# Optimization experiments

Measured on AMD Instinct MI355X. Metric: run time of the kernel, lower is better.

The kernel has to match this reference:

```python
import jax, jax.numpy as jnp
import numpy as np

B, N, OBS, H, A = 1024, 64, 128, 256, 16
NH = 4
HD = H // NH


def _linear_params(key, fan_in, fan_out):
    k1, k2 = jax.random.split(key)
    bound = 1.0 / np.sqrt(fan_in)
    W = jax.random.uniform(k1, (fan_out, fan_in), jnp.float32, -bound, bound)
    b = jax.random.uniform(k2, (fan_out,), jnp.float32, -bound, bound)
    return W, b


def setup_inputs() -> dict:
    key = jax.random.key(0)
    ks = jax.random.split(key, 10)
    obs = jax.random.normal(ks[0], (B, N, OBS), jnp.float32)
    adj = jax.random.randint(ks[1], (B, N, N), 0, 2).astype(jnp.float32)
    # guarantee every row has at least one neighbor (self-loop) so softmax is finite
    adj = jnp.maximum(adj, jnp.eye(N, dtype=jnp.float32)[None])
    W1, b1 = _linear_params(ks[2], OBS, H)
    W2, b2 = _linear_params(ks[3], H, H)
    Wq, bq = _linear_params(ks[4], H, H)
    Wk, bk = _linear_params(ks[5], H, H)
    Wv, bv = _linear_params(ks[6], H, H)
    Wo, bo = _linear_params(ks[7], H, H)
    Wc, bc = _linear_params(ks[8], H, H)
    W3, b3 = _linear_params(ks[9], H, A)
    return dict(obs=obs, adj=adj, W1=W1, b1=b1, W2=W2, b2=b2,
                Wq=Wq, bq=bq, Wk=Wk, bk=bk, Wv=Wv, bv=bv,
                Wo=Wo, bo=bo, Wc=Wc, bc=bc, W3=W3, b3=b3)


def reference(obs, adj, W1, b1, W2, b2, Wq, bq, Wk, bk, Wv, bv, Wo, bo, Wc, bc, W3, b3):
    lin = lambda x, W, b: jnp.einsum('bnd,od->bno', x, W) + b
    x = jax.nn.relu(lin(obs, W1, b1))
    x = jax.nn.relu(lin(x, W2, b2))
    # multi-head attention with adjacency mask
    def heads(t):  # [B,N,H] -> [B,NH,N,HD]
        return t.reshape(B, N, NH, HD).transpose(0, 2, 1, 3)
    q = heads(lin(x, Wq, bq))
    k = heads(lin(x, Wk, bk))
    v = heads(lin(x, Wv, bv))
    scores = jnp.einsum('bhqd,bhkd->bhqk', q, k) / np.sqrt(HD).astype(np.float32)
    scores = jnp.where(adj[:, None] == 0, -jnp.inf, scores)
    attn = jax.nn.softmax(scores, axis=-1)
    out = jnp.einsum('bhqk,bhkd->bhqd', attn, v)
    out = out.transpose(0, 2, 1, 3).reshape(B, N, H)
    x = lin(out, Wo, bo)
    # communication: adj @ fc(x)
    x = jnp.einsum('bnm,bmh->bnh', adj, lin(x, Wc, bc))
    return lin(x, W3, b3)
```

## Files before the change

kernel.cpp:

```cpp
#include <hip/hip_runtime.h>
#include <stdint.h>

typedef unsigned short u16;
typedef unsigned long long u64;
typedef __attribute__((ext_vector_type(8))) short short8;
typedef __attribute__((ext_vector_type(4))) float f32x4;

#define MFMA16 __builtin_amdgcn_mfma_f32_16x16x32_bf16

#define B_ 1024
#define N_ 64
#define MTOT (B_ * N_)

__device__ __forceinline__ u16 f2bf(float f) {
  union { float f; uint32_t u; } v; v.f = f;
  uint32_t r = v.u + 0x7FFFu + ((v.u >> 16) & 1u);
  return (u16)(r >> 16);
}

union U8 { short8 v; u16 u[8]; };
union U4 { u64 v; u16 u[4]; };

__device__ __forceinline__ void cp16(const void* g, void* l) {
  __builtin_amdgcn_global_load_lds(
      (const __attribute__((address_space(1))) void*)g,
      (__attribute__((address_space(3))) void*)l, 16, 0, 0);
}

__global__ __launch_bounds__(256) void k_l1(
    const float* __restrict__ obs, u16* __restrict__ obsb,
    const float* __restrict__ Wc, const float* __restrict__ Wo,
    const float* __restrict__ bo, const float* __restrict__ bc,
    float* __restrict__ M1, float* __restrict__ bv,
    const float* __restrict__ W1, const float* __restrict__ W2,
    const float* __restrict__ Wq, const float* __restrict__ Wk,
    u16* o1, u16* o2, u16* oq, u16* ok) {
  const int bid = blockIdx.x, tid = threadIdx.x;
  if (bid < 4096) {
    const int e = (bid * 256 + tid) * 8;
    f32x4 a = *(const f32x4*)(obs + e);
    f32x4 b = *(const f32x4*)(obs + e + 4);
    U8 pk;
#pragma unroll
    for (int j = 0; j < 4; j++) { pk.u[j] = f2bf(a[j]); pk.u[4 + j] = f2bf(b[j]); }
    *(short8*)(obsb + e) = pk.v;
  } else if (bid < 4352) {
    __shared__ float wcr[256];
    __shared__ float red[4];
    const int j = bid - 4096, d = tid;
    wcr[d] = Wc[j * 256 + d];
    __syncthreads();
    float acc = 0.f;
    for (int i = 0; i < 256; i++) acc += wcr[i] * Wo[i * 256 + d];
    M1[j * 256 + d] = acc;
    float p = wcr[d] * bo[d];
    for (int off = 32; off >= 1; off >>= 1) p += __shfl_xor(p, off);
    if ((d & 63) == 0) red[d >> 6] = p;
    __syncthreads();
    if (d == 0) bv[j] = bc[j] + red[0] + red[1] + red[2] + red[3];
  } else {
    int off8 = (bid - 4352) * 256 + tid;
    const float* src; u16* dst;
    if      (off8 <  4096) { src = W1; dst = o1; }
    else if (off8 < 12288) { src = W2; dst = o2; off8 -= 4096; }
    else if (off8 < 20480) { src = Wq; dst = oq; off8 -= 12288; }
    else                   { src = Wk; dst = ok; off8 -= 20480; }
    const int e = off8 * 8;
    f32x4 a = *(const f32x4*)(src + e);
    f32x4 b = *(const f32x4*)(src + e + 4);
    U8 pk;
#pragma unroll
    for (int j = 0; j < 4; j++) { pk.u[j] = f2bf(a[j]); pk.u[4 + j] = f2bf(b[j]); }
    *(short8*)(dst + e) = pk.v;
  }
}

template<int K>
__device__ __forceinline__ void gemm128t(
    const u16* __restrict__ A, const u16* __restrict__ W,
    const float* __restrict__ bias, u16* __restrict__ C,
    const int m0, const int n0, const bool relu, char* smem) {
  char* As = smem;
  char* Bs = smem + 16384;
  const int tid = threadIdx.x;
  const int lane = tid & 63, wid = tid >> 6;
  const int wr = wid >> 1, wc = wid & 1;
  const int ro = lane & 15, hi = lane >> 4;

  f32x4 acc[4][4];
#pragma unroll
  for (int m = 0; m < 4; m++)
#pragma unroll
    for (int n = 0; n < 4; n++) acc[m][n] = (f32x4){0.f, 0.f, 0.f, 0.f};

  for (int k0 = 0; k0 < K; k0 += 64) {
#pragma unroll
    for (int i = 0; i < 4; i++) {
      const int boff = i * 4096 + wid * 1024;
      const int t = boff + lane * 16;
      const int row = t >> 7;
      const int cb = (t & 127) ^ ((row & 7) << 4);
      cp16(A + (size_t)(m0 + row) * K + k0 + (cb >> 1), As + boff);
    }
#pragma unroll
    for (int i = 0; i < 4; i++) {
      const int boff = i * 4096 + wid * 1024;
      const int t = boff + lane * 16;
      const int row = t >> 7;
      const int cb = (t & 127) ^ ((row & 7) << 4);
      cp16(W + (size_t)(n0 + row) * K + k0 + (cb >> 1), Bs + boff);
    }
    __syncthreads();
#pragma unroll
    for (int kk = 0; kk < 64; kk += 32) {
      short8 af[4], bfr[4];
#pragma unroll
      for (int m = 0; m < 4; m++) {
        const int row = wr * 64 + m * 16 + ro;
        af[m] = *(const short8*)(As + ((row * 128 + (kk + hi * 8) * 2) ^ ((row & 7) << 4)));
      }
#pragma unroll
      for (int n = 0; n < 4; n++) {
        const int row = wc * 64 + n * 16 + ro;
        bfr[n] = *(const short8*)(Bs + ((row * 128 + (kk + hi * 8) * 2) ^ ((row & 7) << 4)));
      }
#pragma unroll
      for (int m = 0; m < 4; m++)
#pragma unroll
        for (int n = 0; n < 4; n++)
          acc[m][n] = MFMA16(af[m], bfr[n], acc[m][n], 0, 0, 0);
    }
    __syncthreads();
  }

  u16 (*Cs)[136] = (u16(*)[136])smem;
#pragma unroll
  for (int half = 0; half < 2; half++) {
    if (wr == half) {
#pragma unroll
      for (int n = 0; n < 4; n++) {
        const int col = wc * 64 + n * 16 + ro;
        const float bb = bias[n0 + col];
#pragma unroll
        for (int m = 0; m < 4; m++)
#pragma unroll
          for (int j = 0; j < 4; j++) {
            float val = acc[m][n][j] + bb;
            if (relu) val = fmaxf(val, 0.f);
            Cs[m * 16 + hi * 4 + j][col] = f2bf(val);
          }
      }
    }
    __syncthreads();
    for (int i = tid; i < 64 * 16; i += 256) {
      const int r = i >> 4, c = (i & 15) << 3;
      *(short8*)(C + (size_t)(m0 + half * 64 + r) * 256 + n0 + c) = *(short8*)&Cs[r][c];
    }
    __syncthreads();
  }
}

__global__ __launch_bounds__(256, 4) void k_gemm1_prep2(
    const u16* __restrict__ obsb, const u16* __restrict__ W1b,
    const float* __restrict__ b1, u16* __restrict__ x1,
    const float* __restrict__ W3, const float* __restrict__ M1,
    const float* __restrict__ bvchain, const float* __restrict__ bvw,
    float* __restrict__ Wzf, float* __restrict__ bz) {
  __shared__ char smem[32768];
  if (blockIdx.x < 1024) {
    gemm128t<128>(obsb, W1b, b1, x1, (int)(blockIdx.x >> 1) * 128,
                  (int)(blockIdx.x & 1) * 128, true, smem);
    return;
  }
  float* w3r = (float*)smem;
  float* red = (float*)(smem + 1024);
  const int a = blockIdx.x - 1024, d = threadIdx.x;
  w3r[d] = W3[a * 256 + d];
  __syncthreads();
  float acc = 0.f;
  for (int j = 0; j < 256; j++) acc += w3r[j] * M1[j * 256 + d];
  Wzf[a * 256 + d] = acc;
  float p = w3r[d] * bvchain[d] + acc * bvw[d];
  for (int off = 32; off >= 1; off >>= 1) p += __shfl_xor(p, off);
  if ((d & 63) == 0) red[d >> 6] = p;
  __syncthreads();
  if (d == 0) bz[a] = red[0] + red[1] + red[2] + red[3];
}

__global__ __launch_bounds__(256, 4) void k_x2_prep3(
    const u16* __restrict__ x1, const u16* __restrict__ W2b,
    const float* __restrict__ b2, u16* __restrict__ x2,
    const float* __restrict__ Wzf, const float* __restrict__ Wv,
    u16* __restrict__ G) {
  __shared__ char smem[32768];
  if (blockIdx.x < 1024) {
    gemm128t<256>(x1, W2b, b2, x2, (int)(blockIdx.x >> 1) * 128,
                  (int)(blockIdx.x & 1) * 128, true, smem);
    return;
  }
  const int g = blockIdx.x - 1024, d2 = threadIdx.x;
  const int h = g >> 4, a = g & 15;
  float* wzr = (float*)smem;
  if (d2 < 64) wzr[d2] = Wzf[a * 256 + h * 64 + d2];
  __syncthreads();
  float acc = 0.f;
#pragma unroll 8
  for (int d = 0; d < 64; d++) acc += wzr[d] * Wv[(size_t)(h * 64 + d) * 256 + d2];
  G[g * 256 + d2] = f2bf(acc);
}

__global__ __launch_bounds__(256, 4) void k_qk_gemmv(
    const u16* __restrict__ x2,
    const u16* __restrict__ Wqb, const float* __restrict__ bq, u16* __restrict__ Qg,
    const u16* __restrict__ Wkb, const float* __restrict__ bk, u16* __restrict__ Kg,
    const u16* __restrict__ G, u16* __restrict__ Vzt) {
  __shared__ char smem[32768];
  const int bid = blockIdx.x;
  if (bid < 2048) {
    const int which = bid & 1;
    gemm128t<256>(x2, which ? Wkb : Wqb, which ? bk : bq, which ? Kg : Qg,
                  (bid >> 2) * 128, ((bid >> 1) & 1) * 128, false, smem);
    return;
  }
  char* As = smem;
  char* Bs = smem + 16384;
  const int tid = threadIdx.x;
  const int lane = tid & 63, w = tid >> 6;
  const int ro = lane & 15, hi = lane >> 4;
  const int m0 = (bid - 2048) * 128;

  f32x4 acc[2][4];
#pragma unroll
  for (int m = 0; m < 2; m++)
#pragma unroll
    for (int n = 0; n < 4; n++) acc[m][n] = (f32x4){0.f, 0.f, 0.f, 0.f};

  for (int k0 = 0; k0 < 256; k0 += 64) {
#pragma unroll
    for (int i = 0; i < 4; i++) {
      const int boff = i * 4096 + w * 1024;
      const int t = boff + lane * 16;
      const int row = t >> 7;
      const int cb = (t & 127) ^ ((row & 7) << 4);
      cp16(x2 + (size_t)(m0 + row) * 256 + k0 + (cb >> 1), As + boff);
    }
    {
      const int boff = w * 1024;
      const int t = boff + lane * 16;
      const int row = t >> 7;
      const int cb = (t & 127) ^ ((row & 7) << 4);
      cp16(G + (size_t)row * 256 + k0 + (cb >> 1), Bs + boff);
      const int boff2 = 4096 + w * 1024;
      const int t2 = boff2 + lane * 16;
      const int row2 = t2 >> 7;
      const int cb2 = (t2 & 127) ^ ((row2 & 7) << 4);
      cp16(G + (size_t)row2 * 256 + k0 + (cb2 >> 1), Bs + boff2);
    }
    __syncthreads();
#pragma unroll
    for (int kk = 0; kk < 64; kk += 32) {
      short8 af[2], bfr[4];
#pragma unroll
      for (int m = 0; m < 2; m++) {
        const int row = w * 32 + m * 16 + ro;
        af[m] = *(const short8*)(As + ((row * 128 + (kk + hi * 8) * 2) ^ ((row & 7) << 4)));
      }
#pragma unroll
      for (int n = 0; n < 4; n++) {
        const int row = n * 16 + ro;
        bfr[n] = *(const short8*)(Bs + ((row * 128 + (kk + hi * 8) * 2) ^ ((row & 7) << 4)));
      }
#pragma unroll
      for (int m = 0; m < 2; m++)
#pragma unroll
        for (int n = 0; n < 4; n++)
          acc[m][n] = MFMA16(af[m], bfr[n], acc[m][n], 0, 0, 0);
    }
    __syncthreads();
  }

#pragma unroll
  for (int m = 0; m < 2; m++) {
    const int rbase = w * 32 + m * 16;
    const int bidx = (m0 >> 6) + (rbase >> 6);
    const int ke = (rbase + hi * 4) & 63;
#pragma unroll
    for (int n = 0; n < 4; n++) {
      const int c = n * 16 + ro;
      U4 pk;
#pragma unroll
      for (int j = 0; j < 4; j++) pk.u[j] = f2bf(acc[m][n][j]);
      *(u64*)(Vzt + (size_t)bidx * 4096 + (size_t)c * 64 + ke) = pk.v;
    }
  }
}

__global__ __launch_bounds__(256, 2) void attn_fused(
    const u16* __restrict__ Qg, const u16* __restrict__ Kg,
    const u16* __restrict__ Vzt, const float* __restrict__ adj,
    const float* __restrict__ bz, const float* __restrict__ b3,
    float* __restrict__ out) {
  __shared__ u16 Ps[4][64][72];
  __shared__ float Zs[4][64][16];
  __shared__ u64 adjm[64];
  __shared__ u16 chunk[64][4];

  const int b = blockIdx.x, tid = threadIdx.x;
  const int lane = tid & 63, w = tid >> 6;
  const int ro = lane & 15, hi = lane >> 4;
  const int hc = w * 64;
  const size_t base = (size_t)b * 64 * 256;

  short8 kb[4][2];
#pragma unroll
  for (int n = 0; n < 4; n++)
#pragma unroll
    for (int ks = 0; ks < 2; ks++)
      kb[n][ks] = *(const short8*)(Kg + base + (size_t)(n * 16 + ro) * 256 + hc + ks * 32 + hi * 8);

  {
    const int q = tid >> 2, qa = tid & 3;
    const float* ar = adj + ((size_t)b * 64 + q) * 64 + qa * 16;
    f32x4 a0 = *(const f32x4*)(ar);
    f32x4 a1 = *(const f32x4*)(ar + 4);
    f32x4 a2 = *(const f32x4*)(ar + 8);
    f32x4 a3 = *(const f32x4*)(ar + 12);
    unsigned m16 = 0;
#pragma unroll
    for (int i = 0; i < 4; i++) {
      m16 |= (unsigned)(a0[i] != 0.f) << i;
      m16 |= (unsigned)(a1[i] != 0.f) << (4 + i);
      m16 |= (unsigned)(a2[i] != 0.f) << (8 + i);
      m16 |= (unsigned)(a3[i] != 0.f) << (12 + i);
    }
    chunk[q][qa] = (u16)m16;
  }

  f32x4 s[4][4];
#pragma unroll
  for (int m = 0; m < 4; m++) {
    short8 af[2];
#pragma unroll
    for (int ks = 0; ks < 2; ks++)
      af[ks] = *(const short8*)(Qg + base + (size_t)(m * 16 + ro) * 256 + hc + ks * 32 + hi * 8);
#pragma unroll
    for (int n = 0; n < 4; n++) s[m][n] = (f32x4){0.f, 0.f, 0.f, 0.f};
#pragma unroll
    for (int ks = 0; ks < 2; ks++)
#pragma unroll
      for (int n = 0; n < 4; n++)
        s[m][n] = MFMA16(af[ks], kb[n][ks], s[m][n], 0, 0, 0);
  }

  short8 vz[2];
#pragma unroll
  for (int ks = 0; ks < 2; ks++)
    vz[ks] = *(const short8*)(Vzt + (size_t)b * 4096 + (size_t)(hc / 4 + ro) * 64 + ks * 32 + hi * 8);

  __syncthreads();
  if (tid < 64)
    adjm[tid] = (u64)chunk[tid][0] | ((u64)chunk[tid][1] << 16) |
                ((u64)chunk[tid][2] << 32) | ((u64)chunk[tid][3] << 48);
  __syncthreads();

#pragma unroll
  for (int m = 0; m < 4; m++) {
#pragma unroll
    for (int j = 0; j < 4; j++) {
      const int q = m * 16 + hi * 4 + j;
      const u64 msk = adjm[q];
      float sv[4], ev[4];
      float mx = -3.0e38f;
#pragma unroll
      for (int n = 0; n < 4; n++) {
        const bool on = (msk >> (n * 16 + ro)) & 1ull;
        sv[n] = on ? s[m][n][j] * 0.125f : -3.0e38f;
        mx = fmaxf(mx, sv[n]);
      }
      mx = fmaxf(mx, __shfl_xor(mx, 1));
      mx = fmaxf(mx, __shfl_xor(mx, 2));
      mx = fmaxf(mx, __shfl_xor(mx, 4));
      mx = fmaxf(mx, __shfl_xor(mx, 8));
      float sum = 0.f;
#pragma unroll
      for (int n = 0; n < 4; n++) {
        ev[n] = (sv[n] > -1.0e37f) ? __expf(sv[n] - mx) : 0.f;
        sum += ev[n];
      }
      sum += __shfl_xor(sum, 1);
      sum += __shfl_xor(sum, 2);
      sum += __shfl_xor(sum, 4);
      sum += __shfl_xor(sum, 8);
      const float inv = 1.0f / sum;
#pragma unroll
      for (int n = 0; n < 4; n++)
        Ps[w][q][n * 16 + ro] = f2bf(ev[n] * inv);
    }
  }

#pragma unroll
  for (int m = 0; m < 4; m++) {
    short8 pa[2];
    pa[0] = *(const short8*)&Ps[w][m * 16 + ro][hi * 8];
    pa[1] = *(const short8*)&Ps[w][m * 16 + ro][32 + hi * 8];
    f32x4 oz = (f32x4){0.f, 0.f, 0.f, 0.f};
#pragma unroll
    for (int ks = 0; ks < 2; ks++)
      oz = MFMA16(pa[ks], vz[ks], oz, 0, 0, 0);
#pragma unroll
    for (int j = 0; j < 4; j++)
      Zs[w][m * 16 + hi * 4 + j][ro] = oz[j];
  }
  __syncthreads();

  for (int i = tid; i < 1024; i += 256) {
    const int r = i >> 4, a = i & 15;
    Zs[0][r][a] += Zs[1][r][a] + Zs[2][r][a] + Zs[3][r][a];
  }
  __syncthreads();

  {
    const int n = tid >> 2, a4 = (tid & 3) << 2;
    const u64 msk = adjm[n];
    const float deg = (float)__popcll(msk);
    float a0 = 0.f, a1 = 0.f, a2 = 0.f, a3 = 0.f;
#pragma unroll 8
    for (int m = 0; m < 64; m++) {
      const float wv = (float)((msk >> m) & 1ull);
      f32x4 z = *(const f32x4*)&Zs[0][m][a4];
      a0 += wv * z[0]; a1 += wv * z[1]; a2 += wv * z[2]; a3 += wv * z[3];
    }
    f32x4 r;
    r[0] = a0 + b3[a4 + 0] + deg * bz[a4 + 0];
    r[1] = a1 + b3[a4 + 1] + deg * bz[a4 + 1];
    r[2] = a2 + b3[a4 + 2] + deg * bz[a4 + 2];
    r[3] = a3 + b3[a4 + 3] + deg * bz[a4 + 3];
    *(f32x4*)(out + ((size_t)b * 64 + n) * 16 + a4) = r;
  }
}

extern "C" void kernel_launch(void* const* d_in, const int* in_sizes, int n_in,
                              void* d_out, int out_size, void* d_ws, size_t ws_size,
                              hipStream_t stream) {
  const float* obs = (const float*)d_in[0];
  const float* adj = (const float*)d_in[1];
  const float* W1  = (const float*)d_in[2];
  const float* b1  = (const float*)d_in[3];
  const float* W2  = (const float*)d_in[4];
  const float* b2  = (const float*)d_in[5];
  const float* Wq  = (const float*)d_in[6];
  const float* bq  = (const float*)d_in[7];
  const float* Wk  = (const float*)d_in[8];
  const float* bk  = (const float*)d_in[9];
  const float* Wv  = (const float*)d_in[10];
  const float* bvw = (const float*)d_in[11];
  const float* Wo  = (const float*)d_in[12];
  const float* bo  = (const float*)d_in[13];
  const float* Wc  = (const float*)d_in[14];
  const float* bc  = (const float*)d_in[15];
  const float* W3  = (const float*)d_in[16];
  const float* b3  = (const float*)d_in[17];
  float* out = (float*)d_out;

  char* ws = (char*)d_ws;
  const size_t BIG = (size_t)MTOT * 256 * 2;
  u16* buf0 = (u16*)(ws);
  u16* buf1 = (u16*)(ws + BIG);
  u16* buf2 = (u16*)(ws + 2 * BIG);
  u16* buf3 = (u16*)(ws + 3 * BIG);
  char* p = ws + 4 * BIG;
  u16* W1b = (u16*)p;              p += 128 * 256 * 2;
  u16* W2b = (u16*)p;              p += 256 * 256 * 2;
  u16* Wqb = (u16*)p;              p += 256 * 256 * 2;
  u16* Wkb = (u16*)p;              p += 256 * 256 * 2;
  float* M1 = (float*)p;           p += 256 * 256 * 4;
  float* Wzf = (float*)p;          p += 16 * 256 * 4;
  u16* G   = (u16*)p;              p += 64 * 256 * 2;
  float* bv = (float*)p;           p += 256 * 4;
  float* bz = (float*)p;           p += 16 * 4;
  u16* obsb = (u16*)p;             p += (size_t)MTOT * 128 * 2;

  dim3 blk(256);
  k_l1<<<dim3(4464), blk, 0, stream>>>(obs, obsb, Wc, Wo, bo, bc, M1, bv,
                                       W1, W2, Wq, Wk, W1b, W2b, Wqb, Wkb);
  k_gemm1_prep2<<<dim3(1040), blk, 0, stream>>>(obsb, W1b, b1, buf0,
                                                W3, M1, bv, bvw, Wzf, bz);
  k_x2_prep3<<<dim3(1088), blk, 0, stream>>>(buf0, W2b, b2, buf1, Wzf, Wv, G);
  k_qk_gemmv<<<dim3(2560), blk, 0, stream>>>(buf1, Wqb, bq, buf2,
                                             Wkb, bk, buf3, G, buf0);
  attn_fused<<<dim3(1024), blk, 0, stream>>>(buf2, buf3, buf0, adj, bz, b3, out);
}
```

Measured before the change: 128.4 us.

## Widen GEMM tiles to full 256-column output so each block reuses the A tile

The bf16 GEMM helper now computes a 128x256 output tile per block, using two accumulator sets and two B tiles in LDS. Previously two blocks each loaded the same A rows for the two column halves. Block counts are halved, LDS per block grows to 48KB and launch bounds drop to 2 blocks per CU to fit the doubled accumulators. The Q/K GEMM blocks are also remapped so that Q and K work on the same row tiles sits close together, for L2 locality. The trade is less A traffic against lower occupancy and fewer blocks to spread across CUs.

```diff
diff --git a/kernel.cpp b/kernel.cpp
--- a/kernel.cpp
+++ b/kernel.cpp
@@ -76,22 +76,26 @@
 }
 
 template<int K>
-__device__ __forceinline__ void gemm128t(
+__device__ __forceinline__ void gemm_full(
     const u16* __restrict__ A, const u16* __restrict__ W,
     const float* __restrict__ bias, u16* __restrict__ C,
-    const int m0, const int n0, const bool relu, char* smem) {
-  char* As = smem;
-  char* Bs = smem + 16384;
+    const int m0, const bool relu, char* smem) {
+  char* As  = smem;
+  char* Bs0 = smem + 16384;
+  char* Bs1 = smem + 32768;
   const int tid = threadIdx.x;
   const int lane = tid & 63, wid = tid >> 6;
   const int wr = wid >> 1, wc = wid & 1;
   const int ro = lane & 15, hi = lane >> 4;
 
-  f32x4 acc[4][4];
+  f32x4 acc0[4][4], acc1[4][4];
 #pragma unroll
   for (int m = 0; m < 4; m++)
 #pragma unroll
-    for (int n = 0; n < 4; n++) acc[m][n] = (f32x4){0.f, 0.f, 0.f, 0.f};
+    for (int n = 0; n < 4; n++) {
+      acc0[m][n] = (f32x4){0.f, 0.f, 0.f, 0.f};
+      acc1[m][n] = (f32x4){0.f, 0.f, 0.f, 0.f};
+    }
 
   for (int k0 = 0; k0 < K; k0 += 64) {
 #pragma unroll
@@ -101,19 +105,13 @@
       const int row = t >> 7;
       const int cb = (t & 127) ^ ((row & 7) << 4);
       cp16(A + (size_t)(m0 + row) * K + k0 + (cb >> 1), As + boff);
-    }
-#pragma unroll
-    for (int i = 0; i < 4; i++) {
-      const int boff = i * 4096 + wid * 1024;
-      const int t = boff + lane * 16;
-      const int row = t >> 7;
-      const int cb = (t & 127) ^ ((row & 7) << 4);
-      cp16(W + (size_t)(n0 + row) * K + k0 + (cb >> 1), Bs + boff);
+      cp16(W + (size_t)row * K + k0 + (cb >> 1), Bs0 + boff);
+      cp16(W + (size_t)(128 + row) * K + k0 + (cb >> 1), Bs1 + boff);
     }
     __syncthreads();
 #pragma unroll
     for (int kk = 0; kk < 64; kk += 32) {
-      short8 af[4], bfr[4];
+      short8 af[4], b0[4], b1[4];
 #pragma unroll
       for (int m = 0; m < 4; m++) {
         const int row = wr * 64 + m * 16 + ro;
@@ -122,59 +120,66 @@
 #pragma unroll
       for (int n = 0; n < 4; n++) {
         const int row = wc * 64 + n * 16 + ro;
-        bfr[n] = *(const short8*)(Bs + ((row * 128 + (kk + hi * 8) * 2) ^ ((row & 7) << 4)));
+        const int off = (row * 128 + (kk + hi * 8) * 2) ^ ((row & 7) << 4);
+        b0[n] = *(const short8*)(Bs0 + off);
+        b1[n] = *(const short8*)(Bs1 + off);
       }
 #pragma unroll
       for (int m = 0; m < 4; m++)
 #pragma unroll
-        for (int n = 0; n < 4; n++)
-          acc[m][n] = MFMA16(af[m], bfr[n], acc[m][n], 0, 0, 0);
+        for (int n = 0; n < 4; n++) {
+          acc0[m][n] = MFMA16(af[m], b0[n], acc0[m][n], 0, 0, 0);
+          acc1[m][n] = MFMA16(af[m], b1[n], acc1[m][n], 0, 0, 0);
+        }
     }
     __syncthreads();
   }
 
   u16 (*Cs)[136] = (u16(*)[136])smem;
-#pragma unroll
-  for (int half = 0; half < 2; half++) {
-    if (wr == half) {
-#pragma unroll
-      for (int n = 0; n < 4; n++) {
-        const int col = wc * 64 + n * 16 + ro;
-        const float bb = bias[n0 + col];
-#pragma unroll
-        for (int m = 0; m < 4; m++)
-#pragma unroll
-          for (int j = 0; j < 4; j++) {
-            float val = acc[m][n][j] + bb;
-            if (relu) val = fmaxf(val, 0.f);
-            Cs[m * 16 + hi * 4 + j][col] = f2bf(val);
-          }
-      }
-    }
-    __syncthreads();
-    for (int i = tid; i < 64 * 16; i += 256) {
-      const int r = i >> 4, c = (i & 15) << 3;
-      *(short8*)(C + (size_t)(m0 + half * 64 + r) * 256 + n0 + c) = *(short8*)&Cs[r][c];
-    }
-    __syncthreads();
-  }
-}
-
-__global__ __launch_bounds__(256, 4) void k_gemm1_prep2(
+  auto ep = [&](f32x4 (&acc)[4][4], const int n0) {
+#pragma unroll
+    for (int half = 0; half < 2; half++) {
+      if (wr == half) {
+#pragma unroll
+        for (int n = 0; n < 4; n++) {
+          const int col = wc * 64 + n * 16 + ro;
+          const float bb = bias[n0 + col];
+#pragma unroll
+          for (int m = 0; m < 4; m++)
+#pragma unroll
+            for (int j = 0; j < 4; j++) {
+              float val = acc[m][n][j] + bb;
+              if (relu) val = fmaxf(val, 0.f);
+              Cs[m * 16 + hi * 4 + j][col] = f2bf(val);
+            }
+        }
+      }
+      __syncthreads();
+      for (int i = tid; i < 64 * 16; i += 256) {
+        const int r = i >> 4, c = (i & 15) << 3;
+        *(short8*)(C + (size_t)(m0 + half * 64 + r) * 256 + n0 + c) = *(short8*)&Cs[r][c];
+      }
+      __syncthreads();
+    }
+  };
+  ep(acc0, 0);
+  ep(acc1, 128);
+}
+
+__global__ __launch_bounds__(256, 2) void k_gemm1_prep2(
     const u16* __restrict__ obsb, const u16* __restrict__ W1b,
     const float* __restrict__ b1, u16* __restrict__ x1,
     const float* __restrict__ W3, const float* __restrict__ M1,
     const float* __restrict__ bvchain, const float* __restrict__ bvw,
     float* __restrict__ Wzf, float* __restrict__ bz) {
-  __shared__ char smem[32768];
-  if (blockIdx.x < 1024) {
-    gemm128t<128>(obsb, W1b, b1, x1, (int)(blockIdx.x >> 1) * 128,
-                  (int)(blockIdx.x & 1) * 128, true, smem);
+  __shared__ char smem[49152];
+  if (blockIdx.x < 512) {
+    gemm_full<128>(obsb, W1b, b1, x1, (int)blockIdx.x * 128, true, smem);
     return;
   }
   float* w3r = (float*)smem;
   float* red = (float*)(smem + 1024);
-  const int a = blockIdx.x - 1024, d = threadIdx.x;
+  const int a = blockIdx.x - 512, d = threadIdx.x;
   w3r[d] = W3[a * 256 + d];
   __syncthreads();
   float acc = 0.f;
@@ -187,18 +192,17 @@
   if (d == 0) bz[a] = red[0] + red[1] + red[2] + red[3];
 }
 
-__global__ __launch_bounds__(256, 4) void k_x2_prep3(
+__global__ __launch_bounds__(256, 2) void k_x2_prep3(
     const u16* __restrict__ x1, const u16* __restrict__ W2b,
     const float* __restrict__ b2, u16* __restrict__ x2,
     const float* __restrict__ Wzf, const float* __restrict__ Wv,
     u16* __restrict__ G) {
-  __shared__ char smem[32768];
-  if (blockIdx.x < 1024) {
-    gemm128t<256>(x1, W2b, b2, x2, (int)(blockIdx.x >> 1) * 128,
-                  (int)(blockIdx.x & 1) * 128, true, smem);
+  __shared__ char smem[49152];
+  if (blockIdx.x < 512) {
+    gemm_full<256>(x1, W2b, b2, x2, (int)blockIdx.x * 128, true, smem);
     return;
   }
-  const int g = blockIdx.x - 1024, d2 = threadIdx.x;
+  const int g = blockIdx.x - 512, d2 = threadIdx.x;
   const int h = g >> 4, a = g & 15;
   float* wzr = (float*)smem;
   if (d2 < 64) wzr[d2] = Wzf[a * 256 + h * 64 + d2];
@@ -209,17 +213,19 @@
   G[g * 256 + d2] = f2bf(acc);
 }
 
-__global__ __launch_bounds__(256, 4) void k_qk_gemmv(
+__global__ __launch_bounds__(256, 2) void k_qk_gemmv(
     const u16* __restrict__ x2,
     const u16* __restrict__ Wqb, const float* __restrict__ bq, u16* __restrict__ Qg,
     const u16* __restrict__ Wkb, const float* __restrict__ bk, u16* __restrict__ Kg,
     const u16* __restrict__ G, u16* __restrict__ Vzt) {
-  __shared__ char smem[32768];
+  __shared__ char smem[49152];
   const int bid = blockIdx.x;
-  if (bid < 2048) {
-    const int which = bid & 1;
-    gemm128t<256>(x2, which ? Wkb : Wqb, which ? bk : bq, which ? Kg : Qg,
-                  (bid >> 2) * 128, ((bid >> 1) & 1) * 128, false, smem);
+  if (bid < 1024) {
+    const int q = bid >> 4, r = bid & 15;
+    const int mt = q * 8 + (r & 7);
+    const int sub = r >> 3;
+    gemm_full<256>(x2, sub ? Wkb : Wqb, sub ? bk : bq, sub ? Kg : Qg,
+                   mt * 128, false, smem);
     return;
   }
   char* As = smem;
@@ -227,7 +233,7 @@
   const int tid = threadIdx.x;
   const int lane = tid & 63, w = tid >> 6;
   const int ro = lane & 15, hi = lane >> 4;
-  const int m0 = (bid - 2048) * 128;
+  const int m0 = (bid - 1024) * 128;
 
   f32x4 acc[2][4];
 #pragma unroll
@@ -483,10 +489,10 @@
   dim3 blk(256);
   k_l1<<<dim3(4464), blk, 0, stream>>>(obs, obsb, Wc, Wo, bo, bc, M1, bv,
                                        W1, W2, Wq, Wk, W1b, W2b, Wqb, Wkb);
-  k_gemm1_prep2<<<dim3(1040), blk, 0, stream>>>(obsb, W1b, b1, buf0,
-                                                W3, M1, bv, bvw, Wzf, bz);
-  k_x2_prep3<<<dim3(1088), blk, 0, stream>>>(buf0, W2b, b2, buf1, Wzf, Wv, G);
-  k_qk_gemmv<<<dim3(2560), blk, 0, stream>>>(buf1, Wqb, bq, buf2,
+  k_gemm1_prep2<<<dim3(528), blk, 0, stream>>>(obsb, W1b, b1, buf0,
+                                               W3, M1, bv, bvw, Wzf, bz);
+  k_x2_prep3<<<dim3(576), blk, 0, stream>>>(buf0, W2b, b2, buf1, Wzf, Wv, G);
+  k_qk_gemmv<<<dim3(1536), blk, 0, stream>>>(buf1, Wqb, bq, buf2,
                                              Wkb, bk, buf3, G, buf0);
   attn_fused<<<dim3(1024), blk, 0, stream>>>(buf2, buf3, buf0, adj, bz, b3, out);
 }
```

Measured after the change: 125.2 us. -2.5%, faster.
